# Performance work log

Measured on AMD Instinct MI355X. Metric: run time of the kernel, lower is better.

The kernel has to match this reference:

```python
import jax, jax.numpy as jnp
from jax import lax
import numpy as np

DIM = 512
NUM_HEADS = 8
SR = 2


def setup_inputs() -> dict:
    key = jax.random.key(0)
    ks = jax.random.split(key, 7)
    B, H, W = 4, 64, 64
    N = H * W
    C = DIM
    s = 0.02
    return {
        "x": jax.random.normal(ks[0], (B, N, C), dtype=jnp.float32),
        "q_w": jax.random.normal(ks[1], (C, C), dtype=jnp.float32) * s,
        "kv_w": jax.random.normal(ks[2], (2 * C, C), dtype=jnp.float32) * s,
        "sr_w": jax.random.normal(ks[3], (C, C, SR, SR), dtype=jnp.float32) * s,
        "sr_b": jax.random.normal(ks[4], (C,), dtype=jnp.float32) * s,
        "proj_w": jax.random.normal(ks[5], (C, C), dtype=jnp.float32) * s,
        "proj_b": jax.random.normal(ks[6], (C,), dtype=jnp.float32) * s,
        "H": H,
        "W": W,
    }


def reference(x, q_w, kv_w, sr_w, sr_b, proj_w, proj_b, H, W):
    B, N, C = x.shape
    nh = NUM_HEADS
    hd = C // nh
    scale = hd ** -0.5

    # q projection: [B, nh, N, hd]
    q = (x @ q_w.T).reshape(B, N, nh, hd).transpose(0, 2, 1, 3)

    # spatial reduction via strided conv (kernel=stride=SR)
    x_ = x.transpose(0, 2, 1).reshape(B, C, H, W)
    x_ = lax.conv_general_dilated(
        x_, sr_w, window_strides=(SR, SR), padding="VALID",
        dimension_numbers=("NCHW", "OIHW", "NCHW"),
    ) + sr_b[None, :, None, None]
    Nk = (H // SR) * (W // SR)
    x_ = x_.reshape(B, C, Nk).transpose(0, 2, 1)  # [B, Nk, C]

    # kv projection: [2, B, nh, Nk, hd]
    kv = (x_ @ kv_w.T).reshape(B, Nk, 2, nh, hd).transpose(2, 0, 3, 1, 4)
    k, v = kv[0], kv[1]

    attn = jax.nn.softmax(jnp.einsum("bhnd,bhmd->bhnm", q, k) * scale, axis=-1)
    out = jnp.einsum("bhnm,bhmd->bhnd", attn, v)  # [B, nh, N, hd]
    out = out.transpose(0, 2, 1, 3).reshape(B, N, C)
    return out @ proj_w.T + proj_b
```

## Files before the change

kernel.cpp:

```cpp
#include <hip/hip_runtime.h>


typedef __attribute__((ext_vector_type(8)))  short short8;
typedef __attribute__((ext_vector_type(8)))  unsigned short ushort8;
typedef __attribute__((ext_vector_type(4)))  float floatx4;
typedef __attribute__((ext_vector_type(16))) float floatx16;

__device__ inline unsigned short bf16r(float f) {
    union { float f; unsigned u; } v; v.f = f;
    unsigned r = v.u + 0x7fffu + ((v.u >> 16) & 1u);
    return (unsigned short)(r >> 16);
}

__device__ inline ushort8 pack8(float4 a, float4 b) {
    ushort8 o;
    o[0] = bf16r(a.x); o[1] = bf16r(a.y); o[2] = bf16r(a.z); o[3] = bf16r(a.w);
    o[4] = bf16r(b.x); o[5] = bf16r(b.y); o[6] = bf16r(b.z); o[7] = bf16r(b.w);
    return o;
}

__device__ inline void gl_lds16(const void* g, void* l) {
    __builtin_amdgcn_global_load_lds(
        (const __attribute__((address_space(1))) unsigned int*)g,
        (__attribute__((address_space(3))) unsigned int*)l, 16, 0, 0);
}

__global__ __launch_bounds__(256)
void prep(const float* __restrict__ x,  const float* __restrict__ qw,
          const float* __restrict__ kvw, const float* __restrict__ srw,
          const float* __restrict__ pw,
          unsigned short* __restrict__ xb,  unsigned short* __restrict__ qwb,
          unsigned short* __restrict__ kvwb, unsigned short* __restrict__ srwb,
          unsigned short* __restrict__ pwb, unsigned short* __restrict__ xrb) {
    const int bid = blockIdx.x;
    if (bid < 5120) {
        const float* src; unsigned short* dst; int off; float sc = 1.f;
        if (bid < 4096)      { src = x;   dst = xb;   off = bid * 256; }
        else if (bid < 4224) { src = qw;  dst = qwb;  off = (bid - 4096) * 256;
                               sc = 0.18033688011112042f;  }
        else if (bid < 4480) { src = kvw; dst = kvwb; off = (bid - 4224) * 256; }
        else if (bid < 4992) { src = srw; dst = srwb; off = (bid - 4480) * 256; }
        else                 { src = pw;  dst = pwb;  off = (bid - 4992) * 256; }
        const int idx = off + threadIdx.x;
        float4 a = *(const float4*)(src + (size_t)idx * 8);
        float4 b = *(const float4*)(src + (size_t)idx * 8 + 4);
        a.x *= sc; a.y *= sc; a.z *= sc; a.w *= sc;
        b.x *= sc; b.y *= sc; b.z *= sc; b.w *= sc;
        *(ushort8*)(dst + (size_t)idx * 8) = pack8(a, b);
    } else {
        const int idx = (bid - 5120) * 256 + threadIdx.x;
        const int c = idx & 511;
        const int m = idx >> 9;
        const int b = m >> 10;
        const int rem = m & 1023;
        const int oi = rem >> 5, oj = rem & 31;
        const int n00 = oi * 128 + oj * 2;
        const float* base = x + ((size_t)b * 4096) * 512 + c;
        const unsigned long long v00 = bf16r(base[(size_t)(n00)      * 512]);
        const unsigned long long v01 = bf16r(base[(size_t)(n00 + 1)  * 512]);
        const unsigned long long v10 = bf16r(base[(size_t)(n00 + 64) * 512]);
        const unsigned long long v11 = bf16r(base[(size_t)(n00 + 65) * 512]);
        const unsigned long long w = v00 | (v01 << 16) | (v10 << 32) | (v11 << 48);
        *(unsigned long long*)(xrb + (size_t)m * 2048 + c * 4) = w;
    }
}

template<int BM, int BN, int MODE>
__global__ __launch_bounds__(256)
void gemm_mfma(const unsigned short* __restrict__ A,
               const unsigned short* __restrict__ B,
               const float* __restrict__ bias,
               float* __restrict__ Cf, unsigned short* __restrict__ Cb,
               int M, int N, int K) {
    constexpr int WR = (BN == 128) ? BM / 2 : BM / 4;
    constexpr int MI = WR / 16;
    __shared__ unsigned short As[BM * 32];
    __shared__ unsigned short Bs[BN * 32];
    const int t = threadIdx.x;
    const int w = t >> 6, l = t & 63;
    const int lq = l & 15, quad = l >> 4;
    const int bm = blockIdx.x * BM, bn = blockIdx.y * BN;
    const int wrow = (BN == 128) ? (w >> 1) * (BM / 2) : w * (BM / 4);
    const int wcol = (BN == 128) ? (w & 1) * 64 : 0;

    floatx4 acc[MI][4];
    #pragma unroll
    for (int mi = 0; mi < MI; ++mi)
        #pragma unroll
        for (int ni = 0; ni < 4; ++ni) acc[mi][ni] = (floatx4){0.f, 0.f, 0.f, 0.f};

    for (int k0 = 0; k0 < K; k0 += 32) {
        __syncthreads();
        #pragma unroll
        for (int i = 0; i < BM / 64; ++i) {
            const int c = i * 256 + t;
            gl_lds16(A + (size_t)(bm + (c >> 2)) * K + k0 + (c & 3) * 8, &As[c * 8]);
        }
        #pragma unroll
        for (int i = 0; i < BN / 64; ++i) {
            const int c = i * 256 + t;
            gl_lds16(B + (size_t)(bn + (c >> 2)) * K + k0 + (c & 3) * 8, &Bs[c * 8]);
        }
        __syncthreads();

        short8 bf[4];
        #pragma unroll
        for (int ni = 0; ni < 4; ++ni)
            bf[ni] = *(const short8*)&Bs[(wcol + ni * 16 + lq) * 32 + quad * 8];
        #pragma unroll
        for (int mi = 0; mi < MI; ++mi) {
            const short8 af = *(const short8*)&As[(wrow + mi * 16 + lq) * 32 + quad * 8];
            #pragma unroll
            for (int ni = 0; ni < 4; ++ni)
                acc[mi][ni] = __builtin_amdgcn_mfma_f32_16x16x32_bf16(
                    af, bf[ni], acc[mi][ni], 0, 0, 0);
        }
    }

    #pragma unroll
    for (int ni = 0; ni < 4; ++ni) {
        const int col = bn + wcol + ni * 16 + lq;
        const float bv = (MODE <= 1 && bias) ? bias[col] : 0.f;
        #pragma unroll
        for (int mi = 0; mi < MI; ++mi) {
            const int row0 = bm + wrow + mi * 16 + quad * 4;
            if (MODE == 0) {
                #pragma unroll
                for (int r = 0; r < 4; ++r)
                    Cf[(size_t)(row0 + r) * N + col] = acc[mi][ni][r] + bv;
            } else if (MODE == 1) {
                unsigned own[4], mg[4];
                #pragma unroll
                for (int r = 0; r < 4; ++r) own[r] = bf16r(acc[mi][ni][r] + bv);
                #pragma unroll
                for (int r = 0; r < 4; ++r) {
                    const unsigned pt = __shfl_xor(own[r], 1);
                    mg[r] = (lq & 1) ? (pt | (own[r] << 16)) : (own[r] | (pt << 16));
                }
                const int colb = bn + wcol + ni * 16 + (lq & ~1);
                const int rb = (lq & 1) * 2;
                *(unsigned*)(Cb + (size_t)(row0 + rb)     * N + colb) = mg[rb];
                *(unsigned*)(Cb + (size_t)(row0 + rb + 1) * N + colb) = mg[rb + 1];
            } else if (MODE == 2) {
                const int kb = col >> 10, key = col & 1023;
                const int h = row0 >> 6, d0 = row0 & 63;
                unsigned long long wv = 0;
                #pragma unroll
                for (int r = 0; r < 4; ++r)
                    wv |= (unsigned long long)bf16r(acc[mi][ni][r]) << (16 * r);
                *(unsigned long long*)(Cb +
                    (((size_t)(kb * 8 + h)) * 1024 + key) * 64 + d0) = wv;
            } else {
                const int kb = row0 >> 10, key0 = row0 & 1023;
                const int h = col >> 6, d = col & 63;
                unsigned long long wv = 0;
                #pragma unroll
                for (int r = 0; r < 4; ++r)
                    wv |= (unsigned long long)bf16r(acc[mi][ni][r]) << (16 * r);
                *(unsigned long long*)(Cb +
                    (((size_t)(kb * 8 + h)) * 64 + d) * 1024 + key0) = wv;
            }
        }
    }
}

#define KS2 72

__global__ __launch_bounds__(256)
void attn_mfma32(const unsigned short* __restrict__ qb,
                 const unsigned short* __restrict__ Kb,
                 const unsigned short* __restrict__ Vt,
                 unsigned short* __restrict__ out) {
    __shared__ unsigned short Ks[64 * KS2];
    __shared__ unsigned short Vs[64 * KS2];

    const int t = threadIdx.x;
    const int w = t >> 6;
    const int lane = t & 63;
    const int m32 = lane & 31;
    const int sig = lane >> 5;
    const int n0 = blockIdx.x * 128;
    const int bh = blockIdx.y;
    const int b = bh >> 3, h = bh & 7;

    short8 qf[4];
    {
        const unsigned short* qrow =
            qb + ((size_t)(b * 4096 + n0 + w * 32 + m32)) * 512 + h * 64;
        #pragma unroll
        for (int kc = 0; kc < 4; ++kc)
            qf[kc] = *(const short8*)(qrow + kc * 16 + sig * 8);
    }

    float l_own = 0.f;
    floatx16 O0, O1;
    #pragma unroll
    for (int i = 0; i < 16; ++i) { O0[i] = 0.f; O1[i] = 0.f; }

    const unsigned short* Kg = Kb + (size_t)bh * 1024 * 64;
    const unsigned short* Vg = Vt + (size_t)bh * 64 * 1024;
    const int srow = t >> 2;
    const int sdb  = (t & 3) * 16;

    for (int kt = 0; kt < 16; ++kt) {
        __syncthreads();
        {
            const unsigned short* src = Kg + ((size_t)(kt * 64 + srow)) * 64 + sdb;
            *(ushort8*)&Ks[srow * KS2 + sdb]     = *(const ushort8*)src;
            *(ushort8*)&Ks[srow * KS2 + sdb + 8] = *(const ushort8*)(src + 8);
        }
        {
            const unsigned short* src = Vg + (size_t)srow * 1024 + kt * 64 + sdb;
            *(ushort8*)&Vs[srow * KS2 + sdb]     = *(const ushort8*)src;
            *(ushort8*)&Vs[srow * KS2 + sdb + 8] = *(const ushort8*)(src + 8);
        }
        __syncthreads();

        floatx16 st0, st1;
        #pragma unroll
        for (int i = 0; i < 16; ++i) { st0[i] = 0.f; st1[i] = 0.f; }
        #pragma unroll
        for (int kc = 0; kc < 4; ++kc) {
            const short8 a0 = *(const short8*)&Ks[m32 * KS2 + kc * 16 + sig * 8];
            st0 = __builtin_amdgcn_mfma_f32_32x32x16_bf16(a0, qf[kc], st0, 0, 0, 0);
            const short8 a1 = *(const short8*)&Ks[(32 + m32) * KS2 + kc * 16 + sig * 8];
            st1 = __builtin_amdgcn_mfma_f32_32x32x16_bf16(a1, qf[kc], st1, 0, 0, 0);
        }

        uint2 E[2][4];
        #pragma unroll
        for (int g = 0; g < 2; ++g) {
            #pragma unroll
            for (int qd = 0; qd < 4; ++qd) {
                const float p0 = __builtin_amdgcn_exp2f(g ? st1[qd * 4 + 0] : st0[qd * 4 + 0]);
                const float p1 = __builtin_amdgcn_exp2f(g ? st1[qd * 4 + 1] : st0[qd * 4 + 1]);
                const float p2 = __builtin_amdgcn_exp2f(g ? st1[qd * 4 + 2] : st0[qd * 4 + 2]);
                const float p3 = __builtin_amdgcn_exp2f(g ? st1[qd * 4 + 3] : st0[qd * 4 + 3]);
                E[g][qd].x = __builtin_amdgcn_perm(
                    __float_as_uint(p1), __float_as_uint(p0), 0x07060302u);
                E[g][qd].y = __builtin_amdgcn_perm(
                    __float_as_uint(p3), __float_as_uint(p2), 0x07060302u);
                l_own += (p0 + p1) + (p2 + p3);
            }
        }

        #pragma unroll
        for (int kc = 0; kc < 4; ++kc) {
            const int g = kc >> 1, qlo = (kc & 1) * 2;
            const uint2 keep = sig ? E[g][qlo + 1] : E[g][qlo];
            const uint2 send = sig ? E[g][qlo]     : E[g][qlo + 1];
            uint2 got;
            got.x = __shfl_xor(send.x, 32);
            got.y = __shfl_xor(send.y, 32);
            uint4 fr;
            fr.x = sig ? got.x  : keep.x;
            fr.y = sig ? got.y  : keep.y;
            fr.z = sig ? keep.x : got.x;
            fr.w = sig ? keep.y : got.y;
            const short8 pa = *(const short8*)&fr;
            const short8 v0 = *(const short8*)&Vs[m32 * KS2 + kc * 16 + sig * 8];
            O0 = __builtin_amdgcn_mfma_f32_32x32x16_bf16(pa, v0, O0, 0, 0, 0);
            const short8 v1 = *(const short8*)&Vs[(32 + m32) * KS2 + kc * 16 + sig * 8];
            O1 = __builtin_amdgcn_mfma_f32_32x32x16_bf16(pa, v1, O1, 0, 0, 0);
        }
    }

    l_own += __shfl_xor(l_own, 32);
    const float inv = 1.0f / l_own;

    float fo0[16], fo1[16];
    #pragma unroll
    for (int r = 0; r < 16; ++r) {
        const float li = __shfl(inv, ((r & 3) + 8 * (r >> 2)) + 4 * sig);
        fo0[r] = O0[r] * li;
        fo1[r] = O1[r] * li;
    }

    #pragma unroll
    for (int gd = 0; gd < 2; ++gd) {
        unsigned mg[16];
        #pragma unroll
        for (int r = 0; r < 16; ++r) {
            const unsigned own = bf16r(gd ? fo1[r] : fo0[r]);
            const unsigned pt = __shfl_xor(own, 1);
            mg[r] = (m32 & 1) ? (pt | (own << 16)) : (own | (pt << 16));
        }
        if ((m32 & 1) == gd) {
            const int colb = h * 64 + gd * 32 + (m32 & ~1);
            #pragma unroll
            for (int r = 0; r < 16; ++r) {
                const int qrow = (r & 3) + 8 * (r >> 2) + 4 * sig;
                const size_t row = (size_t)(b * 4096 + n0 + w * 32 + qrow);
                *(unsigned*)(out + row * 512 + colb) = mg[r];
            }
        }
    }
}

extern "C" void kernel_launch(void* const* d_in, const int* in_sizes, int n_in,
                              void* d_out, int out_size, void* d_ws, size_t ws_size,
                              hipStream_t stream) {
    const float* x      = (const float*)d_in[0];
    const float* q_w    = (const float*)d_in[1];
    const float* kv_w   = (const float*)d_in[2];
    const float* sr_w   = (const float*)d_in[3];
    const float* sr_b   = (const float*)d_in[4];
    const float* proj_w = (const float*)d_in[5];
    const float* proj_b = (const float*)d_in[6];
    float* out = (float*)d_out;

    unsigned short* xb   = (unsigned short*)d_ws;
    unsigned short* attb = xb;
    unsigned short* qb   = xb   + (size_t)16384 * 512;
    unsigned short* xrb  = qb   + (size_t)16384 * 512;
    unsigned short* xsrb = xrb  + (size_t)4096 * 2048;
    unsigned short* qwb  = xsrb + (size_t)4096 * 512;
    unsigned short* kvwb = qwb  + (size_t)512 * 512;
    unsigned short* srwb = kvwb + (size_t)1024 * 512;
    unsigned short* pwb  = srwb + (size_t)512 * 2048;
    unsigned short* Kb   = pwb  + (size_t)512 * 512;
    unsigned short* Vt   = Kb   + (size_t)32 * 1024 * 64;

    const dim3 blk(256);

    prep<<<13312, blk, 0, stream>>>(x, q_w, kv_w, sr_w, proj_w,
                                    xb, qwb, kvwb, srwb, pwb, xrb);

    gemm_mfma<128, 64, 1><<<dim3(128, 8), blk, 0, stream>>>(
        xb, qwb, nullptr, nullptr, qb, 16384, 512, 512);

    gemm_mfma<64, 64, 1><<<dim3(64, 8), blk, 0, stream>>>(
        xrb, srwb, sr_b, nullptr, xsrb, 4096, 512, 2048);

    gemm_mfma<128, 64, 2><<<dim3(4, 64), blk, 0, stream>>>(
        kvwb, xsrb, nullptr, nullptr, Kb, 512, 4096, 512);

    gemm_mfma<128, 64, 3><<<dim3(32, 8), blk, 0, stream>>>(
        xsrb, kvwb + (size_t)512 * 512, nullptr, nullptr, Vt, 4096, 512, 512);

    attn_mfma32<<<dim3(32, 32), blk, 0, stream>>>(qb, Kb, Vt, attb);

    gemm_mfma<128, 64, 0><<<dim3(128, 8), blk, 0, stream>>>(
        attb, pwb, proj_b, out, nullptr, 16384, 512, 512);
}
```

Baseline: 243.3 us.

## Double-buffer GEMM and attention LDS, merge GEMM launches, fuse x conversion passes

The prep kernel now reads x once and writes both the bf16 copy and the 2x2 patch layout. The GEMMs use a K-tile of 64 with XOR-swizzled, double-buffered LDS and setprio around the MFMA work, and the Q and conv GEMMs (and likewise K and V) are merged into single launches. Attention moves to double-buffered swizzled K/V loads through global_load_lds and uses v_permlane32_swap in place of shuffles. The intent is to cut launch count, redundant reads of x, bank conflicts and load stalls, at the cost of more LDS per block and possibly lower occupancy.

```diff
diff --git a/kernel.cpp b/kernel.cpp
--- a/kernel.cpp
+++ b/kernel.cpp
@@ -10,6 +10,13 @@
     union { float f; unsigned u; } v; v.f = f;
     unsigned r = v.u + 0x7fffu + ((v.u >> 16) & 1u);
     return (unsigned short)(r >> 16);
+}
+
+__device__ inline unsigned long long pack4ull(float4 v) {
+    return (unsigned long long)bf16r(v.x)
+         | ((unsigned long long)bf16r(v.y) << 16)
+         | ((unsigned long long)bf16r(v.z) << 32)
+         | ((unsigned long long)bf16r(v.w) << 48);
 }
 
 __device__ inline ushort8 pack8(float4 a, float4 b) {
@@ -33,146 +40,251 @@
           unsigned short* __restrict__ kvwb, unsigned short* __restrict__ srwb,
           unsigned short* __restrict__ pwb, unsigned short* __restrict__ xrb) {
     const int bid = blockIdx.x;
-    if (bid < 5120) {
+    if (bid < 2048) {
+        const int id = bid * 256 + threadIdx.x;
+        const int cq = id & 127, m = id >> 7;
+        const int c0 = cq * 4;
+        const int b = m >> 10, rem = m & 1023;
+        const int oi = rem >> 5, oj = rem & 31;
+        const int n00 = oi * 128 + oj * 2;
+        const float* bp = x + ((size_t)(b * 4096 + n00)) * 512 + c0;
+        const float4 r00 = *(const float4*)bp;
+        const float4 r01 = *(const float4*)(bp + 512);
+        const float4 r10 = *(const float4*)(bp + 64 * 512);
+        const float4 r11 = *(const float4*)(bp + 65 * 512);
+        const unsigned long long w00 = pack4ull(r00), w01 = pack4ull(r01),
+                                 w10 = pack4ull(r10), w11 = pack4ull(r11);
+        unsigned short* xo = xb + ((size_t)(b * 4096 + n00)) * 512 + c0;
+        *(unsigned long long*)(xo)            = w00;
+        *(unsigned long long*)(xo + 512)      = w01;
+        *(unsigned long long*)(xo + 64 * 512) = w10;
+        *(unsigned long long*)(xo + 65 * 512) = w11;
+        unsigned short* xd = xrb + (size_t)m * 2048 + c0 * 4;
+        #pragma unroll
+        for (int j = 0; j < 4; ++j) {
+            const unsigned long long e =
+                  ((w00 >> (16 * j)) & 0xffffull)
+                | (((w01 >> (16 * j)) & 0xffffull) << 16)
+                | (((w10 >> (16 * j)) & 0xffffull) << 32)
+                | (((w11 >> (16 * j)) & 0xffffull) << 48);
+            *(unsigned long long*)(xd + j * 4) = e;
+        }
+    } else {
+        const int b2 = bid - 2048;
         const float* src; unsigned short* dst; int off; float sc = 1.f;
-        if (bid < 4096)      { src = x;   dst = xb;   off = bid * 256; }
-        else if (bid < 4224) { src = qw;  dst = qwb;  off = (bid - 4096) * 256;
-                               sc = 0.18033688011112042f;  }
-        else if (bid < 4480) { src = kvw; dst = kvwb; off = (bid - 4224) * 256; }
-        else if (bid < 4992) { src = srw; dst = srwb; off = (bid - 4480) * 256; }
-        else                 { src = pw;  dst = pwb;  off = (bid - 4992) * 256; }
+        if (b2 < 128)      { src = qw;  dst = qwb;  off = b2 * 256;
+                             sc = 0.18033688011112042f;  }
+        else if (b2 < 384) { src = kvw; dst = kvwb; off = (b2 - 128) * 256; }
+        else if (b2 < 896) { src = srw; dst = srwb; off = (b2 - 384) * 256; }
+        else               { src = pw;  dst = pwb;  off = (b2 - 896) * 256; }
         const int idx = off + threadIdx.x;
         float4 a = *(const float4*)(src + (size_t)idx * 8);
-        float4 b = *(const float4*)(src + (size_t)idx * 8 + 4);
+        float4 bq = *(const float4*)(src + (size_t)idx * 8 + 4);
         a.x *= sc; a.y *= sc; a.z *= sc; a.w *= sc;
-        b.x *= sc; b.y *= sc; b.z *= sc; b.w *= sc;
-        *(ushort8*)(dst + (size_t)idx * 8) = pack8(a, b);
-    } else {
-        const int idx = (bid - 5120) * 256 + threadIdx.x;
-        const int c = idx & 511;
-        const int m = idx >> 9;
-        const int b = m >> 10;
-        const int rem = m & 1023;
-        const int oi = rem >> 5, oj = rem & 31;
-        const int n00 = oi * 128 + oj * 2;
-        const float* base = x + ((size_t)b * 4096) * 512 + c;
-        const unsigned long long v00 = bf16r(base[(size_t)(n00)      * 512]);
-        const unsigned long long v01 = bf16r(base[(size_t)(n00 + 1)  * 512]);
-        const unsigned long long v10 = bf16r(base[(size_t)(n00 + 64) * 512]);
-        const unsigned long long v11 = bf16r(base[(size_t)(n00 + 65) * 512]);
-        const unsigned long long w = v00 | (v01 << 16) | (v10 << 32) | (v11 << 48);
-        *(unsigned long long*)(xrb + (size_t)m * 2048 + c * 4) = w;
-    }
-}
-
-template<int BM, int BN, int MODE>
+        bq.x *= sc; bq.y *= sc; bq.z *= sc; bq.w *= sc;
+        *(ushort8*)(dst + (size_t)idx * 8) = pack8(a, bq);
+    }
+}
+
+__device__ __forceinline__ void g_stage(
+        const unsigned short* __restrict__ A, const unsigned short* __restrict__ B,
+        int K, int bm, int bn, int k0, int t,
+        unsigned short* AsB, unsigned short* BsB) {
+    #pragma unroll
+    for (int i = 0; i < 4; ++i) {
+        const int c = i * 256 + t;
+        const int r = c >> 3, ch = c & 7;
+        gl_lds16(A + (size_t)(bm + r) * K + k0 + ((ch ^ (r & 7)) * 8), AsB + c * 8);
+    }
+    #pragma unroll
+    for (int i = 0; i < 2; ++i) {
+        const int c = i * 256 + t;
+        const int r = c >> 3, ch = c & 7;
+        gl_lds16(B + (size_t)(bn + r) * K + k0 + ((ch ^ (r & 7)) * 8), BsB + c * 8);
+    }
+}
+
+__device__ __forceinline__ void g_comp(
+        const unsigned short* AsB, const unsigned short* BsB,
+        int lq, int quad, int wrow, floatx4 (&acc)[2][4]) {
+    short8 bf[2][4];
+    #pragma unroll
+    for (int kc = 0; kc < 2; ++kc)
+        #pragma unroll
+        for (int ni = 0; ni < 4; ++ni) {
+            const int r = ni * 16 + lq;
+            bf[kc][ni] = *(const short8*)&BsB[r * 64 + (((kc * 4 + quad) ^ (r & 7)) * 8)];
+        }
+    #pragma unroll
+    for (int mi = 0; mi < 2; ++mi) {
+        const int r = wrow + mi * 16 + lq;
+        #pragma unroll
+        for (int kc = 0; kc < 2; ++kc) {
+            const short8 af = *(const short8*)&AsB[r * 64 + (((kc * 4 + quad) ^ (r & 7)) * 8)];
+            #pragma unroll
+            for (int ni = 0; ni < 4; ++ni)
+                acc[mi][ni] = __builtin_amdgcn_mfma_f32_16x16x32_bf16(
+                    af, bf[kc][ni], acc[mi][ni], 0, 0, 0);
+        }
+    }
+}
+
+__device__ __forceinline__ void g_run(
+        const unsigned short* __restrict__ A, const unsigned short* __restrict__ B,
+        int K, int bm, int bn, int t, int lq, int quad, int wrow,
+        unsigned short (&As)[2][128 * 64], unsigned short (&Bs)[2][64 * 64],
+        floatx4 (&acc)[2][4]) {
+    g_stage(A, B, K, bm, bn, 0, t, As[0], Bs[0]);
+    __syncthreads();
+    const int nk = K >> 6;
+    for (int ks = 0; ks < nk; ++ks) {
+        const int cur = ks & 1;
+        if (ks + 1 < nk)
+            g_stage(A, B, K, bm, bn, (ks + 1) * 64, t, As[cur ^ 1], Bs[cur ^ 1]);
+        __builtin_amdgcn_s_setprio(1);
+        g_comp(As[cur], Bs[cur], lq, quad, wrow, acc);
+        __builtin_amdgcn_s_setprio(0);
+        if (ks + 1 < nk) __syncthreads();
+    }
+}
+
 __global__ __launch_bounds__(256)
-void gemm_mfma(const unsigned short* __restrict__ A,
-               const unsigned short* __restrict__ B,
-               const float* __restrict__ bias,
-               float* __restrict__ Cf, unsigned short* __restrict__ Cb,
-               int M, int N, int K) {
-    constexpr int WR = (BN == 128) ? BM / 2 : BM / 4;
-    constexpr int MI = WR / 16;
-    __shared__ unsigned short As[BM * 32];
-    __shared__ unsigned short Bs[BN * 32];
+void gemm_qc(const unsigned short* __restrict__ xb, const unsigned short* __restrict__ qwb,
+             const unsigned short* __restrict__ xrb, const unsigned short* __restrict__ srwb,
+             const float* __restrict__ sr_b,
+             unsigned short* __restrict__ qb, unsigned short* __restrict__ xsrb) {
+    __shared__ unsigned short As[2][128 * 64];
+    __shared__ unsigned short Bs[2][64 * 64];
     const int t = threadIdx.x;
     const int w = t >> 6, l = t & 63;
     const int lq = l & 15, quad = l >> 4;
-    const int bm = blockIdx.x * BM, bn = blockIdx.y * BN;
-    const int wrow = (BN == 128) ? (w >> 1) * (BM / 2) : w * (BM / 4);
-    const int wcol = (BN == 128) ? (w & 1) * 64 : 0;
-
-    floatx4 acc[MI][4];
-    #pragma unroll
-    for (int mi = 0; mi < MI; ++mi)
+    const int wrow = w * 32;
+    const int bx = blockIdx.x;
+    const unsigned short *A, *B; int K, bm; const float* bias; unsigned short* C;
+    if (bx < 128) { A = xb;  B = qwb;  K = 512;  bm = bx * 128;         bias = nullptr; C = qb;   }
+    else          { A = xrb; B = srwb; K = 2048; bm = (bx - 128) * 128; bias = sr_b;    C = xsrb; }
+    const int bn = blockIdx.y * 64;
+
+    floatx4 acc[2][4];
+    #pragma unroll
+    for (int mi = 0; mi < 2; ++mi)
         #pragma unroll
         for (int ni = 0; ni < 4; ++ni) acc[mi][ni] = (floatx4){0.f, 0.f, 0.f, 0.f};
 
-    for (int k0 = 0; k0 < K; k0 += 32) {
-        __syncthreads();
-        #pragma unroll
-        for (int i = 0; i < BM / 64; ++i) {
-            const int c = i * 256 + t;
-            gl_lds16(A + (size_t)(bm + (c >> 2)) * K + k0 + (c & 3) * 8, &As[c * 8]);
-        }
-        #pragma unroll
-        for (int i = 0; i < BN / 64; ++i) {
-            const int c = i * 256 + t;
-            gl_lds16(B + (size_t)(bn + (c >> 2)) * K + k0 + (c & 3) * 8, &Bs[c * 8]);
-        }
-        __syncthreads();
-
-        short8 bf[4];
-        #pragma unroll
-        for (int ni = 0; ni < 4; ++ni)
-            bf[ni] = *(const short8*)&Bs[(wcol + ni * 16 + lq) * 32 + quad * 8];
-        #pragma unroll
-        for (int mi = 0; mi < MI; ++mi) {
-            const short8 af = *(const short8*)&As[(wrow + mi * 16 + lq) * 32 + quad * 8];
-            #pragma unroll
-            for (int ni = 0; ni < 4; ++ni)
-                acc[mi][ni] = __builtin_amdgcn_mfma_f32_16x16x32_bf16(
-                    af, bf[ni], acc[mi][ni], 0, 0, 0);
-        }
-    }
+    g_run(A, B, K, bm, bn, t, lq, quad, wrow, As, Bs, acc);
 
     #pragma unroll
     for (int ni = 0; ni < 4; ++ni) {
-        const int col = bn + wcol + ni * 16 + lq;
-        const float bv = (MODE <= 1 && bias) ? bias[col] : 0.f;
-        #pragma unroll
-        for (int mi = 0; mi < MI; ++mi) {
+        const int col = bn + ni * 16 + lq;
+        const float bv = bias ? bias[col] : 0.f;
+        #pragma unroll
+        for (int mi = 0; mi < 2; ++mi) {
             const int row0 = bm + wrow + mi * 16 + quad * 4;
-            if (MODE == 0) {
-                #pragma unroll
-                for (int r = 0; r < 4; ++r)
-                    Cf[(size_t)(row0 + r) * N + col] = acc[mi][ni][r] + bv;
-            } else if (MODE == 1) {
-                unsigned own[4], mg[4];
-                #pragma unroll
-                for (int r = 0; r < 4; ++r) own[r] = bf16r(acc[mi][ni][r] + bv);
-                #pragma unroll
-                for (int r = 0; r < 4; ++r) {
-                    const unsigned pt = __shfl_xor(own[r], 1);
-                    mg[r] = (lq & 1) ? (pt | (own[r] << 16)) : (own[r] | (pt << 16));
-                }
-                const int colb = bn + wcol + ni * 16 + (lq & ~1);
-                const int rb = (lq & 1) * 2;
-                *(unsigned*)(Cb + (size_t)(row0 + rb)     * N + colb) = mg[rb];
-                *(unsigned*)(Cb + (size_t)(row0 + rb + 1) * N + colb) = mg[rb + 1];
-            } else if (MODE == 2) {
+            unsigned own[4], mg[4];
+            #pragma unroll
+            for (int r = 0; r < 4; ++r) own[r] = bf16r(acc[mi][ni][r] + bv);
+            #pragma unroll
+            for (int r = 0; r < 4; ++r) {
+                const unsigned pt = __shfl_xor(own[r], 1);
+                mg[r] = (lq & 1) ? (pt | (own[r] << 16)) : (own[r] | (pt << 16));
+            }
+            const int colb = bn + ni * 16 + (lq & ~1);
+            const int rb = (lq & 1) * 2;
+            *(unsigned*)(C + (size_t)(row0 + rb)     * 512 + colb) = mg[rb];
+            *(unsigned*)(C + (size_t)(row0 + rb + 1) * 512 + colb) = mg[rb + 1];
+        }
+    }
+}
+
+__global__ __launch_bounds__(256)
+void gemm_kv(const unsigned short* __restrict__ kvwb, const unsigned short* __restrict__ xsrb,
+             unsigned short* __restrict__ Kb, unsigned short* __restrict__ Vt) {
+    __shared__ unsigned short As[2][128 * 64];
+    __shared__ unsigned short Bs[2][64 * 64];
+    const int t = threadIdx.x;
+    const int w = t >> 6, l = t & 63;
+    const int lq = l & 15, quad = l >> 4;
+    const int wrow = w * 32;
+    const int id = blockIdx.x;
+    const bool isK = id < 256;
+    const unsigned short* A = isK ? kvwb : xsrb;
+    const unsigned short* B = isK ? xsrb : kvwb + (size_t)512 * 512;
+    const int bm = isK ? (id & 3) * 128 : ((id - 256) >> 3) * 128;
+    const int bn = isK ? (id >> 2) * 64 : ((id - 256) & 7) * 64;
+
+    floatx4 acc[2][4];
+    #pragma unroll
+    for (int mi = 0; mi < 2; ++mi)
+        #pragma unroll
+        for (int ni = 0; ni < 4; ++ni) acc[mi][ni] = (floatx4){0.f, 0.f, 0.f, 0.f};
+
+    g_run(A, B, 512, bm, bn, t, lq, quad, wrow, As, Bs, acc);
+
+    #pragma unroll
+    for (int ni = 0; ni < 4; ++ni) {
+        const int col = bn + ni * 16 + lq;
+        #pragma unroll
+        for (int mi = 0; mi < 2; ++mi) {
+            const int row0 = bm + wrow + mi * 16 + quad * 4;
+            unsigned long long wv = 0;
+            #pragma unroll
+            for (int r = 0; r < 4; ++r)
+                wv |= (unsigned long long)bf16r(acc[mi][ni][r]) << (16 * r);
+            if (isK) {
                 const int kb = col >> 10, key = col & 1023;
                 const int h = row0 >> 6, d0 = row0 & 63;
-                unsigned long long wv = 0;
-                #pragma unroll
-                for (int r = 0; r < 4; ++r)
-                    wv |= (unsigned long long)bf16r(acc[mi][ni][r]) << (16 * r);
-                *(unsigned long long*)(Cb +
+                *(unsigned long long*)(Kb +
                     (((size_t)(kb * 8 + h)) * 1024 + key) * 64 + d0) = wv;
             } else {
                 const int kb = row0 >> 10, key0 = row0 & 1023;
                 const int h = col >> 6, d = col & 63;
-                unsigned long long wv = 0;
-                #pragma unroll
-                for (int r = 0; r < 4; ++r)
-                    wv |= (unsigned long long)bf16r(acc[mi][ni][r]) << (16 * r);
-                *(unsigned long long*)(Cb +
+                *(unsigned long long*)(Vt +
                     (((size_t)(kb * 8 + h)) * 64 + d) * 1024 + key0) = wv;
             }
         }
     }
 }
 
-#define KS2 72
+__global__ __launch_bounds__(256)
+void gemm_proj(const unsigned short* __restrict__ attb, const unsigned short* __restrict__ pwb,
+               const float* __restrict__ pb, float* __restrict__ out) {
+    __shared__ unsigned short As[2][128 * 64];
+    __shared__ unsigned short Bs[2][64 * 64];
+    const int t = threadIdx.x;
+    const int w = t >> 6, l = t & 63;
+    const int lq = l & 15, quad = l >> 4;
+    const int wrow = w * 32;
+    const int bm = blockIdx.x * 128, bn = blockIdx.y * 64;
+
+    floatx4 acc[2][4];
+    #pragma unroll
+    for (int mi = 0; mi < 2; ++mi)
+        #pragma unroll
+        for (int ni = 0; ni < 4; ++ni) acc[mi][ni] = (floatx4){0.f, 0.f, 0.f, 0.f};
+
+    g_run(attb, pwb, 512, bm, bn, t, lq, quad, wrow, As, Bs, acc);
+
+    #pragma unroll
+    for (int ni = 0; ni < 4; ++ni) {
+        const int col = bn + ni * 16 + lq;
+        const float bv = pb[col];
+        #pragma unroll
+        for (int mi = 0; mi < 2; ++mi) {
+            const int row0 = bm + wrow + mi * 16 + quad * 4;
+            #pragma unroll
+            for (int r = 0; r < 4; ++r)
+                out[(size_t)(row0 + r) * 512 + col] = acc[mi][ni][r] + bv;
+        }
+    }
+}
 
 __global__ __launch_bounds__(256)
 void attn_mfma32(const unsigned short* __restrict__ qb,
                  const unsigned short* __restrict__ Kb,
                  const unsigned short* __restrict__ Vt,
                  unsigned short* __restrict__ out) {
-    __shared__ unsigned short Ks[64 * KS2];
-    __shared__ unsigned short Vs[64 * KS2];
+    __shared__ unsigned short Ks[2][64 * 64];
+    __shared__ unsigned short Vs[2][64 * 64];
 
     const int t = threadIdx.x;
     const int w = t >> 6;
@@ -199,33 +311,47 @@
 
     const unsigned short* Kg = Kb + (size_t)bh * 1024 * 64;
     const unsigned short* Vg = Vt + (size_t)bh * 64 * 1024;
-    const int srow = t >> 2;
-    const int sdb  = (t & 3) * 16;
+
+    #pragma unroll
+    for (int i = 0; i < 2; ++i) {
+        const int c = i * 256 + t;
+        const int r = c >> 3, ch = c & 7;
+        const int sw = (ch ^ (r & 7)) * 8;
+        gl_lds16(Kg + (size_t)r * 64 + sw, &Ks[0][c * 8]);
+        gl_lds16(Vg + (size_t)r * 1024 + sw, &Vs[0][c * 8]);
+    }
+    __syncthreads();
 
     for (int kt = 0; kt < 16; ++kt) {
-        __syncthreads();
-        {
-            const unsigned short* src = Kg + ((size_t)(kt * 64 + srow)) * 64 + sdb;
-            *(ushort8*)&Ks[srow * KS2 + sdb]     = *(const ushort8*)src;
-            *(ushort8*)&Ks[srow * KS2 + sdb + 8] = *(const ushort8*)(src + 8);
-        }
-        {
-            const unsigned short* src = Vg + (size_t)srow * 1024 + kt * 64 + sdb;
-            *(ushort8*)&Vs[srow * KS2 + sdb]     = *(const ushort8*)src;
-            *(ushort8*)&Vs[srow * KS2 + sdb + 8] = *(const ushort8*)(src + 8);
-        }
-        __syncthreads();
+        const int cur = kt & 1;
+        if (kt < 15) {
+            #pragma unroll
+            for (int i = 0; i < 2; ++i) {
+                const int c = i * 256 + t;
+                const int r = c >> 3, ch = c & 7;
+                const int sw = (ch ^ (r & 7)) * 8;
+                gl_lds16(Kg + ((size_t)((kt + 1) * 64 + r)) * 64 + sw,
+                         &Ks[cur ^ 1][c * 8]);
+                gl_lds16(Vg + (size_t)r * 1024 + (kt + 1) * 64 + sw,
+                         &Vs[cur ^ 1][c * 8]);
+            }
+        }
+        const unsigned short* KsC = Ks[cur];
+        const unsigned short* VsC = Vs[cur];
 
         floatx16 st0, st1;
         #pragma unroll
         for (int i = 0; i < 16; ++i) { st0[i] = 0.f; st1[i] = 0.f; }
+        __builtin_amdgcn_s_setprio(1);
         #pragma unroll
         for (int kc = 0; kc < 4; ++kc) {
-            const short8 a0 = *(const short8*)&Ks[m32 * KS2 + kc * 16 + sig * 8];
+            const int swo = (((kc * 2 + sig) ^ (m32 & 7)) * 8);
+            const short8 a0 = *(const short8*)&KsC[m32 * 64 + swo];
             st0 = __builtin_amdgcn_mfma_f32_32x32x16_bf16(a0, qf[kc], st0, 0, 0, 0);
-            const short8 a1 = *(const short8*)&Ks[(32 + m32) * KS2 + kc * 16 + sig * 8];
+            const short8 a1 = *(const short8*)&KsC[(32 + m32) * 64 + swo];
             st1 = __builtin_amdgcn_mfma_f32_32x32x16_bf16(a1, qf[kc], st1, 0, 0, 0);
         }
+        __builtin_amdgcn_s_setprio(0);
 
         uint2 E[2][4];
         #pragma unroll
@@ -247,22 +373,22 @@
         #pragma unroll
         for (int kc = 0; kc < 4; ++kc) {
             const int g = kc >> 1, qlo = (kc & 1) * 2;
-            const uint2 keep = sig ? E[g][qlo + 1] : E[g][qlo];
-            const uint2 send = sig ? E[g][qlo]     : E[g][qlo + 1];
-            uint2 got;
-            got.x = __shfl_xor(send.x, 32);
-            got.y = __shfl_xor(send.y, 32);
-            uint4 fr;
-            fr.x = sig ? got.x  : keep.x;
-            fr.y = sig ? got.y  : keep.y;
-            fr.z = sig ? keep.x : got.x;
-            fr.w = sig ? keep.y : got.y;
+            unsigned ax = E[g][qlo].x, bx_ = E[g][qlo + 1].x;
+            unsigned ay = E[g][qlo].y, by_ = E[g][qlo + 1].y;
+            asm("v_permlane32_swap_b32 %0, %1" : "+v"(ax), "+v"(bx_));
+            asm("v_permlane32_swap_b32 %0, %1" : "+v"(ay), "+v"(by_));
+            uint4 fr; fr.x = ax; fr.y = ay; fr.z = bx_; fr.w = by_;
             const short8 pa = *(const short8*)&fr;
-            const short8 v0 = *(const short8*)&Vs[m32 * KS2 + kc * 16 + sig * 8];
+            const int swo = (((kc * 2 + sig) ^ (m32 & 7)) * 8);
+            __builtin_amdgcn_s_setprio(1);
+            const short8 v0 = *(const short8*)&VsC[m32 * 64 + swo];
             O0 = __builtin_amdgcn_mfma_f32_32x32x16_bf16(pa, v0, O0, 0, 0, 0);
-            const short8 v1 = *(const short8*)&Vs[(32 + m32) * KS2 + kc * 16 + sig * 8];
+            const short8 v1 = *(const short8*)&VsC[(32 + m32) * 64 + swo];
             O1 = __builtin_amdgcn_mfma_f32_32x32x16_bf16(pa, v1, O1, 0, 0, 0);
-        }
+            __builtin_amdgcn_s_setprio(0);
+        }
+
+        if (kt < 15) __syncthreads();
     }
 
     l_own += __shfl_xor(l_own, 32);
@@ -323,23 +449,14 @@
 
     const dim3 blk(256);
 
-    prep<<<13312, blk, 0, stream>>>(x, q_w, kv_w, sr_w, proj_w,
-                                    xb, qwb, kvwb, srwb, pwb, xrb);
-
-    gemm_mfma<128, 64, 1><<<dim3(128, 8), blk, 0, stream>>>(
-        xb, qwb, nullptr, nullptr, qb, 16384, 512, 512);
-
-    gemm_mfma<64, 64, 1><<<dim3(64, 8), blk, 0, stream>>>(
-        xrb, srwb, sr_b, nullptr, xsrb, 4096, 512, 2048);
-
-    gemm_mfma<128, 64, 2><<<dim3(4, 64), blk, 0, stream>>>(
-        kvwb, xsrb, nullptr, nullptr, Kb, 512, 4096, 512);
-
-    gemm_mfma<128, 64, 3><<<dim3(32, 8), blk, 0, stream>>>(
-        xsrb, kvwb + (size_t)512 * 512, nullptr, nullptr, Vt, 4096, 512, 512);
+    prep<<<3072, blk, 0, stream>>>(x, q_w, kv_w, sr_w, proj_w,
+                                   xb, qwb, kvwb, srwb, pwb, xrb);
+
+    gemm_qc<<<dim3(160, 8), blk, 0, stream>>>(xb, qwb, xrb, srwb, sr_b, qb, xsrb);
+
+    gemm_kv<<<512, blk, 0, stream>>>(kvwb, xsrb, Kb, Vt);
 
     attn_mfma32<<<dim3(32, 32), blk, 0, stream>>>(qb, Kb, Vt, attb);
 
-    gemm_mfma<128, 64, 0><<<dim3(128, 8), blk, 0, stream>>>(
-        attb, pwb, proj_b, out, nullptr, 16384, 512, 512);
-}
+    gemm_proj<<<dim3(128, 8), blk, 0, stream>>>(attb, pwb, proj_b, out);
+}
```

Result: faster. 221.9 us (-8.8%).
